# Optimization experiments

Measured on AMD Instinct MI355X. Metric: run time of the kernel, lower is better.

Reference implementation:

```python
import jax, jax.numpy as jnp
import numpy as np

REG_MAX = 16
NUM_CLASSES = 30
IMG_SIZE = 320.0


def make_anchors(strides=(8, 16, 32), feats_shapes=((40, 40), (20, 20), (10, 10))):
    pts = []
    for stride, (h, w) in zip(strides, feats_shapes):
        sx = np.arange(w, dtype=np.float32) + 0.5
        sy = np.arange(h, dtype=np.float32) + 0.5
        gy, gx = np.meshgrid(sy, sx, indexing='ij')
        pts.append(np.stack((gx, gy), -1).reshape(-1, 2) * stride)
    return jnp.asarray(np.concatenate(pts, 0))  # [2100, 2]


def setup_inputs() -> dict:
    key = jax.random.key(0)
    k1, k2, k3, k4 = jax.random.split(key, 4)
    B, M = 128, 50
    pred = jax.random.normal(k1, (B, 4 * REG_MAX + NUM_CLASSES, 2100), dtype=jnp.float32)
    targets_cls = jax.random.randint(k2, (B, M), 0, NUM_CLASSES, dtype=jnp.int32)
    targets_xy = jax.random.uniform(k3, (B, M, 2), dtype=jnp.float32)  # normalized centers
    valid = jax.random.randint(k4, (B, M), 0, 2) > 0  # bool GT-validity mask
    anchors = make_anchors()
    return {"pred": pred, "targets_cls": targets_cls, "targets_xy": targets_xy,
            "valid": valid, "anchors": anchors}


def reference(pred, targets_cls, targets_xy, valid, anchors):
    B = pred.shape[0]
    A = anchors.shape[0]  # 2100
    pred_dist = pred[:, :4 * REG_MAX, :]   # [B, 64, A]
    pred_cls = pred[:, 4 * REG_MAX:, :]    # [B, C, A]

    # --- vectorized nearest-anchor assignment (replaces nested python loops) ---
    centers = targets_xy * IMG_SIZE                               # [B, M, 2]
    dist = jnp.linalg.norm(anchors[None, None, :, :] - centers[:, :, None, :], axis=-1)  # [B, M, A]
    best = jnp.argmin(dist, axis=-1)                              # [B, M]

    b_idx = jnp.broadcast_to(jnp.arange(B)[:, None], best.shape)  # [B, M]
    fg_mask = jnp.zeros((B, A), dtype=bool).at[b_idx, best].max(valid)
    target_cls = jnp.zeros_like(pred_cls).at[b_idx, targets_cls, best].max(
        valid.astype(pred_cls.dtype))

    # --- BCEWithLogits, mean over all elements ---
    loss_cls = jnp.mean(-(target_cls * jax.nn.log_sigmoid(pred_cls)
                          + (1.0 - target_cls) * jax.nn.log_sigmoid(-pred_cls)))

    # --- Huber(delta=1) on pred_dist.mean(dim=1)[fg_mask] vs 1.0, mean over fg ---
    m = pred_dist.mean(axis=1)            # [B, A]
    e = m - 1.0
    huber = jnp.where(jnp.abs(e) <= 1.0, 0.5 * e * e, jnp.abs(e) - 0.5)
    cnt = fg_mask.sum().astype(pred.dtype)
    loss_box = jnp.where(cnt > 0,
                         (huber * fg_mask.astype(pred.dtype)).sum() / jnp.maximum(cnt, 1.0),
                         jnp.zeros((), pred.dtype))
    return (loss_box, loss_cls)
```

## Files before the change

### kernel.cpp

```cpp
#include <hip/hip_runtime.h>
#include <cfloat>
#include <cmath>

#define BB 128
#define MM 50
#define AA 2100
#define NC 30
#define DCH 64
#define CHT 94
#define GPB 525
#define LOSS_BLOCK 128
#define LOSS_GRID ((BB * GPB) / LOSS_BLOCK)

__global__ void assign_kernel(const float* __restrict__ txy,
                              const int* __restrict__ tcls,
                              const unsigned char* __restrict__ valid,
                              const float* __restrict__ anchors,
                              unsigned int* __restrict__ codes,
                              double* __restrict__ sums,
                              unsigned int* __restrict__ cnt,
                              unsigned int* __restrict__ ticket) {
    int gtid = blockIdx.x * blockDim.x + threadIdx.x;
    if (gtid == 0) { sums[0] = 0.0; sums[1] = 0.0; *cnt = 0u; *ticket = 0u; }
    int pair = gtid >> 6;
    int lane = gtid & 63;
    if (pair >= BB * MM) return;
    if (!valid[pair]) {
        if (lane == 0) codes[pair] = 0xFFFFFFFFu;
        return;
    }

    float cx = txy[pair * 2 + 0] * 320.0f;
    float cy = txy[pair * 2 + 1] * 320.0f;

    const float2* __restrict__ anc = (const float2*)anchors;
    float bd = FLT_MAX;
    int   bi = 0x7fffffff;
    #pragma unroll 4
    for (int a = lane; a < AA; a += 64) {
        float2 p = anc[a];
        float dx = p.x - cx;
        float dy = p.y - cy;
        float d = dx * dx + dy * dy;
        if (d < bd) { bd = d; bi = a; }
    }
    for (int off = 32; off > 0; off >>= 1) {
        float od = __shfl_xor(bd, off);
        int   oi = __shfl_xor(bi, off);
        if (od < bd || (od == bd && oi < bi)) { bd = od; bi = oi; }
    }
    if (lane == 0)
        codes[pair] = (unsigned int)bi | ((unsigned int)tcls[pair] << 16);
}

__device__ __forceinline__ float huber_of_mean(float s) {
    float e = s * (1.0f / 64.0f) - 1.0f;
    float ae = fabsf(e);
    return (ae <= 1.0f) ? 0.5f * e * e : ae - 0.5f;
}

__global__ __launch_bounds__(LOSS_BLOCK)
void loss_kernel(const float* __restrict__ pred,
                 const unsigned int* __restrict__ codes,
                 double* __restrict__ sums,
                 unsigned int* __restrict__ cnt,
                 unsigned int* __restrict__ ticket,
                 float* __restrict__ out) {
    int idx = blockIdx.x * LOSS_BLOCK + threadIdx.x;
    int b = idx / GPB;
    int g = idx - b * GPB;
    int a0 = g * 4;
    const float* __restrict__ pb = pred + (size_t)b * CHT * AA;

    const float* __restrict__ pc = pb + (size_t)DCH * AA + a0;
    float4 xs[NC];
    #pragma unroll
    for (int c = 0; c < NC; ++c)
        xs[c] = *(const float4*)(pc + (size_t)c * AA);

    unsigned int mw0 = 0, mw1 = 0, mw2 = 0, mw3 = 0;
    const unsigned int* __restrict__ cb = codes + b * MM;
    #pragma unroll 5
    for (int m = 0; m < MM; ++m) {
        unsigned int code = cb[m];
        if (code != 0xFFFFFFFFu) {
            int best = (int)(code & 0xFFFFu);
            unsigned int bit = (1u << (code >> 16)) | 0x80000000u;
            unsigned int d = (unsigned int)(best - a0);
            if (d < 4u) {
                if (d == 0u) mw0 |= bit;
                else if (d == 1u) mw1 |= bit;
                else if (d == 2u) mw2 |= bit;
                else mw3 |= bit;
            }
        }
    }

    float acc = 0.0f;
    #pragma unroll
    for (int c = 0; c < NC; ++c) {
        float4 v = xs[c];
        float sp;
        sp = fmaxf(v.x, 0.f) + __logf(1.f + __expf(-fabsf(v.x)));
        acc += sp - (((mw0 >> c) & 1u) ? v.x : 0.f);
        sp = fmaxf(v.y, 0.f) + __logf(1.f + __expf(-fabsf(v.y)));
        acc += sp - (((mw1 >> c) & 1u) ? v.y : 0.f);
        sp = fmaxf(v.z, 0.f) + __logf(1.f + __expf(-fabsf(v.z)));
        acc += sp - (((mw2 >> c) & 1u) ? v.z : 0.f);
        sp = fmaxf(v.w, 0.f) + __logf(1.f + __expf(-fabsf(v.w)));
        acc += sp - (((mw3 >> c) & 1u) ? v.w : 0.f);
    }

    float box = 0.0f;
    unsigned int nfg = 0;
    if ((mw0 | mw1 | mw2 | mw3) & 0x80000000u) {
        float4 s = make_float4(0.f, 0.f, 0.f, 0.f);
        #pragma unroll 8
        for (int ch = 0; ch < DCH; ++ch) {
            float4 v = *(const float4*)(pb + (size_t)ch * AA + a0);
            s.x += v.x; s.y += v.y; s.z += v.z; s.w += v.w;
        }
        if (mw0 >> 31) { box += huber_of_mean(s.x); nfg++; }
        if (mw1 >> 31) { box += huber_of_mean(s.y); nfg++; }
        if (mw2 >> 31) { box += huber_of_mean(s.z); nfg++; }
        if (mw3 >> 31) { box += huber_of_mean(s.w); nfg++; }
    }

    for (int off = 32; off > 0; off >>= 1) {
        acc += __shfl_down(acc, off);
        box += __shfl_down(box, off);
        nfg += __shfl_down(nfg, off);
    }
    __shared__ float s_cls[2];
    __shared__ float s_box[2];
    __shared__ unsigned int s_fg[2];
    int lane = threadIdx.x & 63;
    int w = threadIdx.x >> 6;
    if (lane == 0) { s_cls[w] = acc; s_box[w] = box; s_fg[w] = nfg; }
    __syncthreads();

    if (threadIdx.x == 0) {
        atomicAdd(&sums[0], (double)((double)s_cls[0] + (double)s_cls[1]));
        atomicAdd(&sums[1], (double)((double)s_box[0] + (double)s_box[1]));
        unsigned int tf = s_fg[0] + s_fg[1];
        if (tf) atomicAdd(cnt, tf);
        __threadfence();
        unsigned int old = atomicAdd(ticket, 1u);
        if (old == (unsigned int)(LOSS_GRID - 1)) {
            double tc = atomicAdd(&sums[0], 0.0);
            double tb = atomicAdd(&sums[1], 0.0);
            unsigned int c = atomicAdd(cnt, 0u);
            out[0] = (c > 0) ? (float)(tb / (double)c) : 0.0f;
            out[1] = (float)(tc / (double)((size_t)BB * NC * AA));
        }
    }
}

extern "C" void kernel_launch(void* const* d_in, const int* in_sizes, int n_in,
                              void* d_out, int out_size, void* d_ws, size_t ws_size,
                              hipStream_t stream) {
    const float*         pred    = (const float*)d_in[0];
    const int*           tcls    = (const int*)d_in[1];
    const float*         txy     = (const float*)d_in[2];
    const unsigned char* valid   = (const unsigned char*)d_in[3];
    const float*         anchors = (const float*)d_in[4];
    float* out = (float*)d_out;

    double*       sums   = (double*)d_ws;
    unsigned int* cnt    = (unsigned int*)((char*)d_ws + 16);
    unsigned int* ticket = (unsigned int*)((char*)d_ws + 20);
    unsigned int* codes  = (unsigned int*)((char*)d_ws + 24);

    {
        int threads = BB * MM * 64;
        int block = 256;
        int grid = (threads + block - 1) / block;
        assign_kernel<<<grid, block, 0, stream>>>(txy, tcls, valid, anchors,
                                                  codes, sums, cnt, ticket);
    }
    loss_kernel<<<LOSS_GRID, LOSS_BLOCK, 0, stream>>>(pred, codes, sums, cnt,
                                                      ticket, out);
}
```

Before: 199.8 us.

## Split class channels across two threads and spread atomics over slots

Each 4-anchor group is now handled by two threads, each covering 15 of the 30 class channels. This doubles the thread count and cuts per-thread register pressure for the preloaded logits. The block grows to 256 threads, and per-block partial sums go to 64 striped double slots instead of one address, which reduces contention on the global atomics. The last block reduces the slots. The trade-off is that the code words are scanned twice per anchor group and the block now has an extra sync.

```diff
diff --git a/kernel.cpp b/kernel.cpp
--- a/kernel.cpp
+++ b/kernel.cpp
@@ -9,19 +9,25 @@
 #define DCH 64
 #define CHT 94
 #define GPB 525
-#define LOSS_BLOCK 128
-#define LOSS_GRID ((BB * GPB) / LOSS_BLOCK)
+#define TOTG (BB * GPB)
+#define HCLS 15
+#define LOSS_BLOCK 256
+#define LOSS_GRID ((2 * TOTG) / LOSS_BLOCK)
+#define NSLOT 64
 
 __global__ void assign_kernel(const float* __restrict__ txy,
                               const int* __restrict__ tcls,
                               const unsigned char* __restrict__ valid,
                               const float* __restrict__ anchors,
                               unsigned int* __restrict__ codes,
-                              double* __restrict__ sums,
-                              unsigned int* __restrict__ cnt,
+                              double* __restrict__ pcls,
+                              double* __restrict__ pbox,
+                              unsigned int* __restrict__ pcnt,
                               unsigned int* __restrict__ ticket) {
     int gtid = blockIdx.x * blockDim.x + threadIdx.x;
-    if (gtid == 0) { sums[0] = 0.0; sums[1] = 0.0; *cnt = 0u; *ticket = 0u; }
+    if (gtid < NSLOT) { pcls[gtid] = 0.0; pbox[gtid] = 0.0; pcnt[gtid] = 0u; }
+    if (gtid == 0) *ticket = 0u;
+
     int pair = gtid >> 6;
     int lane = gtid & 63;
     if (pair >= BB * MM) return;
@@ -62,20 +68,24 @@
 __global__ __launch_bounds__(LOSS_BLOCK)
 void loss_kernel(const float* __restrict__ pred,
                  const unsigned int* __restrict__ codes,
-                 double* __restrict__ sums,
-                 unsigned int* __restrict__ cnt,
+                 double* __restrict__ pcls,
+                 double* __restrict__ pbox,
+                 unsigned int* __restrict__ pcnt,
                  unsigned int* __restrict__ ticket,
                  float* __restrict__ out) {
-    int idx = blockIdx.x * LOSS_BLOCK + threadIdx.x;
-    int b = idx / GPB;
-    int g = idx - b * GPB;
+    int tid = blockIdx.x * LOSS_BLOCK + threadIdx.x;
+    int h  = tid / TOTG;
+    int gi = tid - h * TOTG;
+    int b  = gi / GPB;
+    int g  = gi - b * GPB;
     int a0 = g * 4;
+    int c0 = h * HCLS;
     const float* __restrict__ pb = pred + (size_t)b * CHT * AA;
 
-    const float* __restrict__ pc = pb + (size_t)DCH * AA + a0;
-    float4 xs[NC];
+    const float* __restrict__ pc = pb + (size_t)(DCH + c0) * AA + a0;
+    float4 xs[HCLS];
     #pragma unroll
-    for (int c = 0; c < NC; ++c)
+    for (int c = 0; c < HCLS; ++c)
         xs[c] = *(const float4*)(pc + (size_t)c * AA);
 
     unsigned int mw0 = 0, mw1 = 0, mw2 = 0, mw3 = 0;
@@ -84,10 +94,11 @@
     for (int m = 0; m < MM; ++m) {
         unsigned int code = cb[m];
         if (code != 0xFFFFFFFFu) {
-            int best = (int)(code & 0xFFFFu);
-            unsigned int bit = (1u << (code >> 16)) | 0x80000000u;
-            unsigned int d = (unsigned int)(best - a0);
+            unsigned int d = (code & 0xFFFFu) - (unsigned int)a0;
             if (d < 4u) {
+                int cc = (int)(code >> 16) - c0;
+                unsigned int bit = 0x80000000u |
+                    ((cc >= 0 && cc < HCLS) ? (1u << cc) : 0u);
                 if (d == 0u) mw0 |= bit;
                 else if (d == 1u) mw1 |= bit;
                 else if (d == 2u) mw2 |= bit;
@@ -96,9 +107,24 @@
         }
     }
 
+    float box = 0.0f;
+    unsigned int nfg = 0;
+    if (h == 0 && ((mw0 | mw1 | mw2 | mw3) >> 31)) {
+        float4 s = make_float4(0.f, 0.f, 0.f, 0.f);
+        #pragma unroll 8
+        for (int ch = 0; ch < DCH; ++ch) {
+            float4 v = *(const float4*)(pb + (size_t)ch * AA + a0);
+            s.x += v.x; s.y += v.y; s.z += v.z; s.w += v.w;
+        }
+        if (mw0 >> 31) { box += huber_of_mean(s.x); nfg++; }
+        if (mw1 >> 31) { box += huber_of_mean(s.y); nfg++; }
+        if (mw2 >> 31) { box += huber_of_mean(s.z); nfg++; }
+        if (mw3 >> 31) { box += huber_of_mean(s.w); nfg++; }
+    }
+
     float acc = 0.0f;
     #pragma unroll
-    for (int c = 0; c < NC; ++c) {
+    for (int c = 0; c < HCLS; ++c) {
         float4 v = xs[c];
         float sp;
         sp = fmaxf(v.x, 0.f) + __logf(1.f + __expf(-fabsf(v.x)));
@@ -111,47 +137,46 @@
         acc += sp - (((mw3 >> c) & 1u) ? v.w : 0.f);
     }
 
-    float box = 0.0f;
-    unsigned int nfg = 0;
-    if ((mw0 | mw1 | mw2 | mw3) & 0x80000000u) {
-        float4 s = make_float4(0.f, 0.f, 0.f, 0.f);
-        #pragma unroll 8
-        for (int ch = 0; ch < DCH; ++ch) {
-            float4 v = *(const float4*)(pb + (size_t)ch * AA + a0);
-            s.x += v.x; s.y += v.y; s.z += v.z; s.w += v.w;
-        }
-        if (mw0 >> 31) { box += huber_of_mean(s.x); nfg++; }
-        if (mw1 >> 31) { box += huber_of_mean(s.y); nfg++; }
-        if (mw2 >> 31) { box += huber_of_mean(s.z); nfg++; }
-        if (mw3 >> 31) { box += huber_of_mean(s.w); nfg++; }
-    }
-
     for (int off = 32; off > 0; off >>= 1) {
         acc += __shfl_down(acc, off);
         box += __shfl_down(box, off);
         nfg += __shfl_down(nfg, off);
     }
-    __shared__ float s_cls[2];
-    __shared__ float s_box[2];
-    __shared__ unsigned int s_fg[2];
+    __shared__ float s_cls[4];
+    __shared__ float s_box[4];
+    __shared__ unsigned int s_fg[4];
+    __shared__ int is_last;
     int lane = threadIdx.x & 63;
     int w = threadIdx.x >> 6;
     if (lane == 0) { s_cls[w] = acc; s_box[w] = box; s_fg[w] = nfg; }
     __syncthreads();
 
     if (threadIdx.x == 0) {
-        atomicAdd(&sums[0], (double)((double)s_cls[0] + (double)s_cls[1]));
-        atomicAdd(&sums[1], (double)((double)s_box[0] + (double)s_box[1]));
-        unsigned int tf = s_fg[0] + s_fg[1];
-        if (tf) atomicAdd(cnt, tf);
+        int slot = blockIdx.x & (NSLOT - 1);
+        double tc = (double)s_cls[0] + s_cls[1] + s_cls[2] + s_cls[3];
+        double tb = (double)s_box[0] + s_box[1] + s_box[2] + s_box[3];
+        unsigned int tf = s_fg[0] + s_fg[1] + s_fg[2] + s_fg[3];
+        atomicAdd(&pcls[slot], tc);
+        if (tb != 0.0) atomicAdd(&pbox[slot], tb);
+        if (tf) atomicAdd(&pcnt[slot], tf);
         __threadfence();
         unsigned int old = atomicAdd(ticket, 1u);
-        if (old == (unsigned int)(LOSS_GRID - 1)) {
-            double tc = atomicAdd(&sums[0], 0.0);
-            double tb = atomicAdd(&sums[1], 0.0);
-            unsigned int c = atomicAdd(cnt, 0u);
-            out[0] = (c > 0) ? (float)(tb / (double)c) : 0.0f;
-            out[1] = (float)(tc / (double)((size_t)BB * NC * AA));
+        is_last = (old == (unsigned int)(LOSS_GRID - 1));
+    }
+    __syncthreads();
+
+    if (is_last && threadIdx.x < NSLOT) {
+        double cs = atomicAdd(&pcls[threadIdx.x], 0.0);
+        double bs = atomicAdd(&pbox[threadIdx.x], 0.0);
+        unsigned int ct = atomicAdd(&pcnt[threadIdx.x], 0u);
+        for (int off = 32; off > 0; off >>= 1) {
+            cs += __shfl_down(cs, off);
+            bs += __shfl_down(bs, off);
+            ct += __shfl_down(ct, off);
+        }
+        if (threadIdx.x == 0) {
+            out[0] = (ct > 0) ? (float)(bs / (double)ct) : 0.0f;
+            out[1] = (float)(cs / (double)((size_t)BB * NC * AA));
         }
     }
 }
@@ -166,18 +191,19 @@
     const float*         anchors = (const float*)d_in[4];
     float* out = (float*)d_out;
 
-    double*       sums   = (double*)d_ws;
-    unsigned int* cnt    = (unsigned int*)((char*)d_ws + 16);
-    unsigned int* ticket = (unsigned int*)((char*)d_ws + 20);
-    unsigned int* codes  = (unsigned int*)((char*)d_ws + 24);
+    double*       pcls   = (double*)d_ws;
+    double*       pbox   = (double*)((char*)d_ws + 512);
+    unsigned int* pcnt   = (unsigned int*)((char*)d_ws + 1024);
+    unsigned int* ticket = (unsigned int*)((char*)d_ws + 1280);
+    unsigned int* codes  = (unsigned int*)((char*)d_ws + 1536);
 
     {
         int threads = BB * MM * 64;
         int block = 256;
         int grid = (threads + block - 1) / block;
         assign_kernel<<<grid, block, 0, stream>>>(txy, tcls, valid, anchors,
-                                                  codes, sums, cnt, ticket);
-    }
-    loss_kernel<<<LOSS_GRID, LOSS_BLOCK, 0, stream>>>(pred, codes, sums, cnt,
-                                                      ticket, out);
-}
+                                                  codes, pcls, pbox, pcnt, ticket);
+    }
+    loss_kernel<<<LOSS_GRID, LOSS_BLOCK, 0, stream>>>(pred, codes, pcls, pbox,
+                                                      pcnt, ticket, out);
+}
```

Measured after the change: 168.9 us. -15.5%, faster.
